# Kernel optimization log

Hardware: AMD Instinct MI355X
Metric: run time of the kernel (lower is better)

Reference implementation:

```python
import jax, jax.numpy as jnp
import numpy as np

B, T, D = 4, 4096, 1024
H = 16
DK = D // H
EPS = 1e-6


def _phi(x):
    return jax.nn.elu(x) + 1.0


def setup_inputs() -> dict:
    key = jax.random.key(0)
    ks = jax.random.split(key, 9)
    s = 1.0 / np.sqrt(D)
    return {
        "x": jax.random.normal(ks[0], (B, T, D), dtype=jnp.float32),
        "Wq": jax.random.uniform(ks[1], (D, D), jnp.float32, -s, s),
        "bq": jax.random.uniform(ks[2], (D,), jnp.float32, -s, s),
        "Wk": jax.random.uniform(ks[3], (D, D), jnp.float32, -s, s),
        "bk": jax.random.uniform(ks[4], (D,), jnp.float32, -s, s),
        "Wv": jax.random.uniform(ks[5], (D, D), jnp.float32, -s, s),
        "bv": jax.random.uniform(ks[6], (D,), jnp.float32, -s, s),
        "Wo": jax.random.uniform(ks[7], (D, D), jnp.float32, -s, s),
        "bo": jax.random.uniform(ks[8], (D,), jnp.float32, -s, s),
    }


def reference(x, Wq, bq, Wk, bk, Wv, bv, Wo, bo):
    Bq, Tq, _ = x.shape

    def heads(y):  # [B,T,D] -> [B,H,T,DK]
        return y.reshape(Bq, Tq, H, DK).transpose(0, 2, 1, 3)

    q = _phi(heads(x @ Wq.T + bq))
    k = _phi(heads(x @ Wk.T + bk))
    v = heads(x @ Wv.T + bv)

    # associative KV summary: [B,H,DK,DK]
    kv = jnp.einsum("bhtd,bhtm->bhdm", k, v)
    # normalizer: q . (sum_t k + eps), then +eps, reciprocal
    z = 1.0 / (jnp.einsum("bhtd,bhd->bht", q, k.sum(axis=2) + EPS) + EPS)
    out = jnp.einsum("bhtd,bhdm,bht->bhtm", q, kv, z)

    out = out.transpose(0, 2, 1, 3).reshape(Bq, Tq, -1)  # [B,T,D]
    return out @ Wo.T + bo
```

## Files before the change

kernel.cpp:

```cpp
#include <hip/hip_runtime.h>
#include <cstdint>
#include <cstddef>

typedef unsigned short u16;
typedef __bf16 bf16x8 __attribute__((ext_vector_type(8)));
typedef float  f32x4  __attribute__((ext_vector_type(4)));
typedef u16    u16x8v __attribute__((ext_vector_type(8)));
typedef u16    u16x4  __attribute__((ext_vector_type(4)));

#define EPS 1e-6f

__device__ __forceinline__ u16 f2bf(float f) {
  union { float f; unsigned int u; } v; v.f = f;
  unsigned int u = v.u + 0x7FFFu + ((v.u >> 16) & 1u);
  return (u16)(u >> 16);
}
__device__ __forceinline__ float bf2f(u16 h) {
  union { unsigned int u; float f; } v; v.u = ((unsigned int)h) << 16;
  return v.f;
}
__device__ __forceinline__ void async16(const void* g, void* l) {
  __builtin_amdgcn_global_load_lds(
      (const __attribute__((address_space(1))) void*)g,
      (__attribute__((address_space(3))) void*)l, 16, 0, 0);
}

__global__ __launch_bounds__(256) void cvt_bf16_kernel(
    const float* __restrict__ in, u16* __restrict__ out, int n8) {
  int i = blockIdx.x * 256 + threadIdx.x;
  if (i >= n8) return;
  const float4* p = (const float4*)in;
  float4 a = p[2 * (size_t)i], b = p[2 * (size_t)i + 1];
  u16x8v o;
  o[0] = f2bf(a.x); o[1] = f2bf(a.y); o[2] = f2bf(a.z); o[3] = f2bf(a.w);
  o[4] = f2bf(b.x); o[5] = f2bf(b.y); o[6] = f2bf(b.z); o[7] = f2bf(b.w);
  *(u16x8v*)(out + 8 * (size_t)i) = o;
}

__global__ __launch_bounds__(256) void cvt_w_kernel(
    const float* __restrict__ w0, const float* __restrict__ w1,
    const float* __restrict__ w2, const float* __restrict__ w3,
    u16* __restrict__ o0, u16* __restrict__ o1,
    u16* __restrict__ o2, u16* __restrict__ o3) {
  const int gb = blockIdx.x;
  const float* in = (gb < 512) ? w0 : (gb < 1024) ? w1 : (gb < 1536) ? w2 : w3;
  u16* out = (gb < 512) ? o0 : (gb < 1024) ? o1 : (gb < 1536) ? o2 : o3;
  const int i = (gb & 511) * 256 + threadIdx.x;
  const float4* p = (const float4*)in;
  float4 a = p[2 * (size_t)i], b = p[2 * (size_t)i + 1];
  u16x8v o;
  o[0] = f2bf(a.x); o[1] = f2bf(a.y); o[2] = f2bf(a.z); o[3] = f2bf(a.w);
  o[4] = f2bf(b.x); o[5] = f2bf(b.y); o[6] = f2bf(b.z); o[7] = f2bf(b.w);
  *(u16x8v*)(out + 8 * (size_t)i) = o;
}

template <int MODE>
__global__ __launch_bounds__(512) void gemm8p(
    const u16* __restrict__ A, const u16* __restrict__ Bw,
    const float* __restrict__ bias0, const float* __restrict__ bias1,
    const float* __restrict__ bias2,
    u16* __restrict__ O0, u16* __restrict__ O1, u16* __restrict__ O2,
    float* __restrict__ Of, int K) {
  __shared__ u16 sA[2][256 * 64];
  __shared__ u16 sB[2][256 * 64];

  const int tid = threadIdx.x, wave = tid >> 6, lane = tid & 63;
  const int bm = blockIdx.x * 256, bn = blockIdx.y * 256;
  const int wmh = (wave >> 2) * 64;
  const int wq  = (wave & 3) * 32;
  const int l15 = lane & 15, l4 = lane >> 4, l7 = lane & 7;

  f32x4 acc[8][4] = {};

  const int trow = tid >> 3;
  const int sch8 = ((tid & 7) ^ (trow & 7)) * 8;

#define STG_A(buf, qm, s, kt)                                                 \
  async16(A + (size_t)(bm + (s)*128 + (qm)*64 + trow) * K + (kt) + sch8,      \
          &sA[buf][(((qm)*128 + (s)*64) + wave * 8) * 64])
#define STG_B(buf, qn, s, kt)                                                 \
  async16(Bw + (size_t)(bn + ((s)*2 + (trow >> 5)) * 64 + (qn)*32 +           \
                        (trow & 31)) * K + (kt) + sch8,                       \
          &sB[buf][(((qn)*128 + (s)*64) + wave * 8) * 64])

  bf16x8 af[4][2], bq[2][2];

#define PH_READS(buf, qm, qn)                                                 \
  _Pragma("unroll") for (int m = 0; m < 4; m++)                               \
    _Pragma("unroll") for (int kk = 0; kk < 2; kk++)                          \
      af[m][kk] = *(const bf16x8*)&sA[buf][((qm)*128 + wmh + m * 16 + l15) * 64 \
                                           + ((kk * 4 + l4) ^ l7) * 8];       \
  _Pragma("unroll") for (int n = 0; n < 2; n++)                               \
    _Pragma("unroll") for (int kk = 0; kk < 2; kk++)                          \
      bq[n][kk] = *(const bf16x8*)&sB[buf][((qn)*128 + wq + n * 16 + l15) * 64 \
                                           + ((kk * 4 + l4) ^ l7) * 8];

#define PH_MFMA(qm, qn)                                                       \
  __builtin_amdgcn_s_barrier();                                               \
  asm volatile("s_waitcnt lgkmcnt(0)" ::: "memory");                          \
  __builtin_amdgcn_s_setprio(1);                                              \
  _Pragma("unroll") for (int kk = 0; kk < 2; kk++)                            \
    _Pragma("unroll") for (int m = 0; m < 4; m++)                             \
      _Pragma("unroll") for (int n = 0; n < 2; n++)                           \
        acc[(qm)*4 + m][(qn)*2 + n] = __builtin_amdgcn_mfma_f32_16x16x32_bf16(\
            af[m][kk], bq[n][kk], acc[(qm)*4 + m][(qn)*2 + n], 0, 0, 0);      \
  __builtin_amdgcn_s_setprio(0);                                              \
  __builtin_amdgcn_s_barrier();                                               \
  asm volatile("" ::: "memory");

  STG_A(0, 0, 0, 0);  STG_A(0, 0, 1, 0);
  STG_B(0, 0, 0, 0);  STG_B(0, 0, 1, 0);
  STG_A(0, 1, 0, 0);  STG_A(0, 1, 1, 0);
  STG_B(0, 1, 0, 0);  STG_B(0, 1, 1, 0);
  STG_A(1, 0, 0, 64); STG_A(1, 0, 1, 64);
  STG_B(1, 0, 0, 64); STG_B(1, 0, 1, 64);
  asm volatile("s_waitcnt vmcnt(4)" ::: "memory");
  __builtin_amdgcn_s_barrier();
  asm volatile("" ::: "memory");

  const int NT = K >> 6;
  const int NI = NT >> 1;
  for (int i = 0; i < NI; ++i) {
    const int kO  = (2 * i + 1) * 64;
    const int kE2 = (2 * i + 2) * 64;
    const int kO2 = (2 * i + 3) * 64;
    const bool gE2 = (2 * i + 2) < NT;
    const bool gO2 = (2 * i + 3) < NT;

    PH_READS(0, 0, 0);
    STG_A(1, 1, 0, kO); STG_A(1, 1, 1, kO);
    PH_MFMA(0, 0);
    PH_READS(0, 0, 1);
    STG_B(1, 1, 0, kO); STG_B(1, 1, 1, kO);
    PH_MFMA(0, 1);
    PH_READS(0, 1, 0);
    if (gE2) { STG_A(0, 0, 0, kE2); STG_A(0, 0, 1, kE2); }
    PH_MFMA(1, 0);
    PH_READS(0, 1, 1);
    if (gE2) {
      STG_B(0, 0, 0, kE2); STG_B(0, 0, 1, kE2);
      asm volatile("s_waitcnt vmcnt(4)" ::: "memory");
    } else {
      asm volatile("s_waitcnt vmcnt(0)" ::: "memory");
    }
    PH_MFMA(1, 1);
    PH_READS(1, 0, 0);
    if (gE2) { STG_A(0, 1, 0, kE2); STG_A(0, 1, 1, kE2); }
    PH_MFMA(0, 0);
    PH_READS(1, 0, 1);
    if (gE2) { STG_B(0, 1, 0, kE2); STG_B(0, 1, 1, kE2); }
    PH_MFMA(0, 1);
    PH_READS(1, 1, 0);
    if (gO2) { STG_A(1, 0, 0, kO2); STG_A(1, 0, 1, kO2); }
    PH_MFMA(1, 0);
    PH_READS(1, 1, 1);
    if (gO2) { STG_B(1, 0, 0, kO2); STG_B(1, 0, 1, kO2); }
    asm volatile("s_waitcnt vmcnt(4)" ::: "memory");
    PH_MFMA(1, 1);
  }
#undef STG_A
#undef STG_B
#undef PH_READS
#undef PH_MFMA

  const int wm = wmh * 2;
  const int wn = (wave & 3) * 64;
  const int r0 = l4 * 4, cc = l15;
  if constexpr (MODE == 1) {
    const int mat = blockIdx.y >> 2;
    u16* outp = (mat == 0) ? O0 : (mat == 1) ? O1 : O2;
    const float* bias = (mat == 0) ? bias0 : (mat == 1) ? bias1 : bias2;
    const int act = (mat < 2);
    const int colb = (blockIdx.y & 3) * 256;
    float bvv[4];
#pragma unroll
    for (int ni = 0; ni < 4; ni++) bvv[ni] = bias[colb + wn + ni * 16 + cc];
#pragma unroll
    for (int mi = 0; mi < 8; mi++) {
#pragma unroll
      for (int j = 0; j < 4; j++) {
        const int row = bm + wm + mi * 16 + r0 + j;
#pragma unroll
        for (int ni = 0; ni < 4; ni++) {
          const int col = colb + wn + ni * 16 + cc;
          float val = acc[mi][ni][j] + bvv[ni];
          if (act) val = (val > 0.f) ? (val + 1.f) : __expf(val);
          outp[(size_t)row * 1024 + col] = f2bf(val);
        }
      }
    }
  } else {
    float bvv[4];
#pragma unroll
    for (int ni = 0; ni < 4; ni++) bvv[ni] = bias0[bn + wn + ni * 16 + cc];
#pragma unroll
    for (int mi = 0; mi < 8; mi++) {
#pragma unroll
      for (int j = 0; j < 4; j++) {
        const int row = bm + wm + mi * 16 + r0 + j;
#pragma unroll
        for (int ni = 0; ni < 4; ni++) {
          const int col = bn + wn + ni * 16 + cc;
          Of[(size_t)row * 1024 + col] = acc[mi][ni][j] + bvv[ni];
        }
      }
    }
  }
}

__global__ __launch_bounds__(256) void kv_mfma_kernel(
    const u16* __restrict__ Kb, const u16* __restrict__ Vb,
    float* __restrict__ kv, float* __restrict__ ksum) {
  const int bh = blockIdx.y;
  const int chunk = blockIdx.x;
  const int b = bh >> 4, h = bh & 15;
  const int tid = threadIdx.x, wave = tid >> 6, lane = tid & 63;

  __shared__ u16 sKT[64 * 64];
  __shared__ u16 sVT[64 * 64];

  f32x4 acc[4] = {};
  f32x4 accs[4] = {};

  union { u16x8v u; bf16x8 b; } uo;
#pragma unroll
  for (int e = 0; e < 8; e++) uo.u[e] = 0x3F80;
  const bf16x8 ones = uo.b;

  const int half = tid >> 7;
  const int j    = tid & 127;
  const int tg   = j >> 3;
  const int dg   = j & 7;
  const u16* src = half ? Vb : Kb;
  u16* dst = half ? sVT : sKT;
  const int colb = (4 * tg + 8 * dg) & 63;

  const size_t rowBase = (size_t)b * 4096 + (size_t)chunk * 512;
  const size_t gbase = (rowBase + 4 * tg) * 1024 + (size_t)h * 64 + dg * 8;

  u16x8v pre[2][4];
#pragma unroll
  for (int s = 0; s < 4; s++)
    pre[0][s] = *(const u16x8v*)(src + gbase + (size_t)s * 1024);

#pragma unroll
  for (int st = 0; st < 8; st++) {
    const int cb = st & 1;
    __syncthreads();
#pragma unroll
    for (int e = 0; e < 8; e++) {
      u16x4 w;
      w[0] = pre[cb][0][e]; w[1] = pre[cb][1][e];
      w[2] = pre[cb][2][e]; w[3] = pre[cb][3][e];
      *(u16x4*)&dst[(dg * 8 + e) * 64 + colb] = w;
    }
    if (st + 1 < 8) {
      const size_t nb = gbase + (size_t)(st + 1) * 64 * 1024;
#pragma unroll
      for (int s = 0; s < 4; s++)
        pre[cb ^ 1][s] = *(const u16x8v*)(src + nb + (size_t)s * 1024);
    }
    __syncthreads();

#pragma unroll
    for (int kst = 0; kst < 2; kst++) {
      const int q8 = kst * 32 + (lane >> 4) * 8;
      bf16x8 bfrag;
      {
        const int rr = wave * 16 + (lane & 15);
        const int c = (q8 + 8 * (rr >> 3)) & 63;
        bfrag = *(const bf16x8*)&sVT[rr * 64 + c];
      }
#pragma unroll
      for (int i = 0; i < 4; i++) {
        const int rr = i * 16 + (lane & 15);
        const int c = (q8 + 8 * (rr >> 3)) & 63;
        const bf16x8 afrag = *(const bf16x8*)&sKT[rr * 64 + c];
        acc[i] = __builtin_amdgcn_mfma_f32_16x16x32_bf16(afrag, bfrag, acc[i], 0, 0, 0);
        if (wave == 0)
          accs[i] = __builtin_amdgcn_mfma_f32_16x16x32_bf16(afrag, ones, accs[i], 0, 0, 0);
      }
    }
  }

  const int r0 = (lane >> 4) * 4, cc = lane & 15;
  float* kvp = kv + (size_t)bh * 4096;
#pragma unroll
  for (int i = 0; i < 4; i++)
#pragma unroll
    for (int jj = 0; jj < 4; jj++)
      atomicAdd(&kvp[(size_t)(i * 16 + r0 + jj) * 64 + wave * 16 + cc], acc[i][jj]);
  if (wave == 0 && cc == 0) {
#pragma unroll
    for (int i = 0; i < 4; i++)
#pragma unroll
      for (int jj = 0; jj < 4; jj++)
        atomicAdd(&ksum[(size_t)bh * 64 + i * 16 + r0 + jj], accs[i][jj]);
  }
}

#define QST 80
__global__ __launch_bounds__(256) void attn_apply_kernel(
    const u16* __restrict__ Qb, const float* __restrict__ kv,
    const float* __restrict__ ksum, u16* __restrict__ attn) {
  const int bh = blockIdx.y;
  const int tt = blockIdx.x;
  const int b = bh >> 4, h = bh & 15;
  const int tid = threadIdx.x, wave = tid >> 6, lane = tid & 63;

  __shared__ u16 skvT[64 * QST];
  __shared__ u16 sq[64 * QST];
  __shared__ float sz[64];
  __shared__ float sks[64];

  if (tid < 64) sks[tid] = ksum[(size_t)bh * 64 + tid] + EPS;

  const float* kvp = kv + (size_t)bh * 4096;
  for (int i = tid; i < 4096; i += 256) {
    const int dd = i >> 6, mm = i & 63;
    skvT[mm * QST + dd] = f2bf(kvp[i]);
  }
  const size_t qbase = ((size_t)b * 4096 + (size_t)tt * 64) * 1024 + h * 64;
  for (int i = tid; i < 4096; i += 256) {
    const int r = i >> 6, dd = i & 63;
    sq[r * QST + dd] = Qb[qbase + (size_t)r * 1024 + dd];
  }
  __syncthreads();

  if (tid < 64) {
    float za = 0.f;
#pragma unroll
    for (int j = 0; j < 64; j++) {
      const int dd = (j + tid) & 63;
      za += bf2f(sq[tid * QST + dd]) * sks[dd];
    }
    sz[tid] = 1.f / (za + EPS);
  }
  __syncthreads();

  f32x4 acc[4] = {};
#pragma unroll
  for (int ks2 = 0; ks2 < 2; ks2++) {
    const bf16x8 a = *(const bf16x8*)&sq[(wave * 16 + (lane & 15)) * QST + ks2 * 32 + (lane >> 4) * 8];
#pragma unroll
    for (int ni = 0; ni < 4; ni++) {
      const bf16x8 bv = *(const bf16x8*)&skvT[(ni * 16 + (lane & 15)) * QST + ks2 * 32 + (lane >> 4) * 8];
      acc[ni] = __builtin_amdgcn_mfma_f32_16x16x32_bf16(a, bv, acc[ni], 0, 0, 0);
    }
  }

  const int r0 = (lane >> 4) * 4, cc = lane & 15;
#pragma unroll
  for (int ni = 0; ni < 4; ni++) {
#pragma unroll
    for (int j = 0; j < 4; j++) {
      const int r = wave * 16 + r0 + j;
      const int c = ni * 16 + cc;
      const float val = acc[ni][j] * sz[r];
      attn[qbase + (size_t)r * 1024 + c] = f2bf(val);
    }
  }
}

extern "C" void kernel_launch(void* const* d_in, const int* in_sizes, int n_in,
                              void* d_out, int out_size, void* d_ws, size_t ws_size,
                              hipStream_t stream) {
  (void)in_sizes; (void)n_in; (void)out_size; (void)ws_size;
  const float* x  = (const float*)d_in[0];
  const float* Wq = (const float*)d_in[1];
  const float* bq = (const float*)d_in[2];
  const float* Wk = (const float*)d_in[3];
  const float* bk = (const float*)d_in[4];
  const float* Wv = (const float*)d_in[5];
  const float* bv = (const float*)d_in[6];
  const float* Wo = (const float*)d_in[7];
  const float* bo = (const float*)d_in[8];

  char* ws = (char*)d_ws;
  u16* xb    = (u16*)ws;  ws += 33554432;
  u16* wqkvb = (u16*)ws;  ws += 6291456;
  u16* wob   = (u16*)ws;  ws += 2097152;
  u16* Vb    = (u16*)ws;  ws += 33554432;
  u16* attn  = (u16*)ws;  ws += 33554432;
  float* kvb  = (float*)ws; ws += 1048576;
  float* ksum = (float*)ws; ws += 16384;

  u16* Qb = (u16*)d_out;
  u16* Kb = Qb + 16777216;

  hipMemsetAsync(kvb, 0, 1048576 + 16384, stream);

  cvt_bf16_kernel<<<8192, 256, 0, stream>>>(x, xb, 2097152);
  cvt_w_kernel<<<2048, 256, 0, stream>>>(Wq, Wk, Wv, Wo,
                                         wqkvb, wqkvb + 1048576, wqkvb + 2097152, wob);

  gemm8p<1><<<dim3(64, 12), 512, 0, stream>>>(
      xb, wqkvb, bq, bk, bv, Qb, Kb, Vb, nullptr, 1024);

  kv_mfma_kernel<<<dim3(8, 64), dim3(256), 0, stream>>>(Kb, Vb, kvb, ksum);
  attn_apply_kernel<<<dim3(64, 64), dim3(256), 0, stream>>>(Qb, kvb, ksum, attn);

  gemm8p<0><<<dim3(64, 4), 512, 0, stream>>>(
      attn, wob, bo, nullptr, nullptr, nullptr, nullptr, nullptr,
      (float*)d_out, 1024);
}
```

Before: 338.0 us.

## Restructure GEMM main loop into four phases with full B-fragment reuse

Changes the bf16 MFMA GEMM inner loop from eight phases per double-tile to four. Each phase now loads all four B fragments once and reuses them across a 4x4 MFMA block, which halves the barriers per tile and removes redundant LDS reads of B. Global-to-LDS prefetches are regrouped and the vmcnt waits move into the phase epilogue, with a peeled final iteration that drains the pipeline. It adds sched_barrier and raises register pressure from the larger B fragment set, and the staged-load ordering is fragile if the wait counts do not match.

```diff
diff --git a/kernel.cpp b/kernel.cpp
--- a/kernel.cpp
+++ b/kernel.cpp
@@ -55,7 +55,7 @@
 }
 
 template <int MODE>
-__global__ __launch_bounds__(512) void gemm8p(
+__global__ __launch_bounds__(512) void gemm4p(
     const u16* __restrict__ A, const u16* __restrict__ Bw,
     const float* __restrict__ bias0, const float* __restrict__ bias1,
     const float* __restrict__ bias2,
@@ -83,85 +83,91 @@
                         (trow & 31)) * K + (kt) + sch8,                       \
           &sB[buf][(((qn)*128 + (s)*64) + wave * 8) * 64])
 
-  bf16x8 af[4][2], bq[2][2];
-
-#define PH_READS(buf, qm, qn)                                                 \
+  bf16x8 af[4][2], bq[4][2];
+
+#define RD_A(buf, qm)                                                         \
   _Pragma("unroll") for (int m = 0; m < 4; m++)                               \
     _Pragma("unroll") for (int kk = 0; kk < 2; kk++)                          \
       af[m][kk] = *(const bf16x8*)&sA[buf][((qm)*128 + wmh + m * 16 + l15) * 64 \
-                                           + ((kk * 4 + l4) ^ l7) * 8];       \
-  _Pragma("unroll") for (int n = 0; n < 2; n++)                               \
+                                           + ((kk * 4 + l4) ^ l7) * 8];
+#define RD_B(buf)                                                             \
+  _Pragma("unroll") for (int nf = 0; nf < 4; nf++)                            \
     _Pragma("unroll") for (int kk = 0; kk < 2; kk++)                          \
-      bq[n][kk] = *(const bf16x8*)&sB[buf][((qn)*128 + wq + n * 16 + l15) * 64 \
-                                           + ((kk * 4 + l4) ^ l7) * 8];
-
-#define PH_MFMA(qm, qn)                                                       \
+      bq[nf][kk] = *(const bf16x8*)&sB[buf][((nf >> 1) * 128 + wq +           \
+                                            (nf & 1) * 16 + l15) * 64 +       \
+                                           ((kk * 4 + l4) ^ l7) * 8];
+
+#define WAITV(n) asm volatile("s_waitcnt vmcnt(" #n ")" ::: "memory")
+
+#define PH_EXEC(qm, NW)                                                       \
   __builtin_amdgcn_s_barrier();                                               \
   asm volatile("s_waitcnt lgkmcnt(0)" ::: "memory");                          \
+  __builtin_amdgcn_sched_barrier(0);                                          \
   __builtin_amdgcn_s_setprio(1);                                              \
   _Pragma("unroll") for (int kk = 0; kk < 2; kk++)                            \
     _Pragma("unroll") for (int m = 0; m < 4; m++)                             \
-      _Pragma("unroll") for (int n = 0; n < 2; n++)                           \
-        acc[(qm)*4 + m][(qn)*2 + n] = __builtin_amdgcn_mfma_f32_16x16x32_bf16(\
-            af[m][kk], bq[n][kk], acc[(qm)*4 + m][(qn)*2 + n], 0, 0, 0);      \
+      _Pragma("unroll") for (int nf = 0; nf < 4; nf++)                        \
+        acc[(qm)*4 + m][nf] = __builtin_amdgcn_mfma_f32_16x16x32_bf16(        \
+            af[m][kk], bq[nf][kk], acc[(qm)*4 + m][nf], 0, 0, 0);             \
   __builtin_amdgcn_s_setprio(0);                                              \
+  WAITV(NW);                                                                  \
   __builtin_amdgcn_s_barrier();                                               \
   asm volatile("" ::: "memory");
 
+#define ITER_BODY(kO, kE2, kO2, hasT2, hasT3, W0, W1, W2, W3)                 \
+                                          \
+  RD_B(0); RD_A(0, 0);                                                        \
+  STG_A(1, 1, 0, kO); STG_A(1, 1, 1, kO);               \
+  PH_EXEC(0, W0);                                                             \
+                                                          \
+  RD_A(0, 1);                                                                 \
+  if (hasT2) {                                                                \
+    STG_B(0, 0, 0, kE2); STG_B(0, 0, 1, kE2);                                 \
+    STG_B(0, 1, 0, kE2); STG_B(0, 1, 1, kE2);                       \
+    STG_A(0, 0, 0, kE2); STG_A(0, 0, 1, kE2);                      \
+  }                                                                           \
+  PH_EXEC(1, W1);                                                             \
+                                          \
+  RD_B(1); RD_A(1, 0);                                                        \
+  if (hasT2) { STG_A(0, 1, 0, kE2); STG_A(0, 1, 1, kE2); }         \
+  PH_EXEC(0, W2);                                                             \
+                                                          \
+  RD_A(1, 1);                                                                 \
+  if (hasT3) {                                                                \
+    STG_B(1, 0, 0, kO2); STG_B(1, 0, 1, kO2);                                 \
+    STG_B(1, 1, 0, kO2); STG_B(1, 1, 1, kO2);                       \
+    STG_A(1, 0, 0, kO2); STG_A(1, 0, 1, kO2);                      \
+  }                                                                           \
+  PH_EXEC(1, W3);
+
+  STG_B(0, 0, 0, 0);  STG_B(0, 0, 1, 0);  STG_B(0, 1, 0, 0);  STG_B(0, 1, 1, 0);
   STG_A(0, 0, 0, 0);  STG_A(0, 0, 1, 0);
-  STG_B(0, 0, 0, 0);  STG_B(0, 0, 1, 0);
   STG_A(0, 1, 0, 0);  STG_A(0, 1, 1, 0);
-  STG_B(0, 1, 0, 0);  STG_B(0, 1, 1, 0);
+  STG_B(1, 0, 0, 64); STG_B(1, 0, 1, 64); STG_B(1, 1, 0, 64); STG_B(1, 1, 1, 64);
   STG_A(1, 0, 0, 64); STG_A(1, 0, 1, 64);
-  STG_B(1, 0, 0, 64); STG_B(1, 0, 1, 64);
-  asm volatile("s_waitcnt vmcnt(4)" ::: "memory");
+  WAITV(6);
   __builtin_amdgcn_s_barrier();
   asm volatile("" ::: "memory");
 
   const int NT = K >> 6;
   const int NI = NT >> 1;
-  for (int i = 0; i < NI; ++i) {
+  for (int i = 0; i < NI - 1; ++i) {
     const int kO  = (2 * i + 1) * 64;
     const int kE2 = (2 * i + 2) * 64;
     const int kO2 = (2 * i + 3) * 64;
-    const bool gE2 = (2 * i + 2) < NT;
-    const bool gO2 = (2 * i + 3) < NT;
-
-    PH_READS(0, 0, 0);
-    STG_A(1, 1, 0, kO); STG_A(1, 1, 1, kO);
-    PH_MFMA(0, 0);
-    PH_READS(0, 0, 1);
-    STG_B(1, 1, 0, kO); STG_B(1, 1, 1, kO);
-    PH_MFMA(0, 1);
-    PH_READS(0, 1, 0);
-    if (gE2) { STG_A(0, 0, 0, kE2); STG_A(0, 0, 1, kE2); }
-    PH_MFMA(1, 0);
-    PH_READS(0, 1, 1);
-    if (gE2) {
-      STG_B(0, 0, 0, kE2); STG_B(0, 0, 1, kE2);
-      asm volatile("s_waitcnt vmcnt(4)" ::: "memory");
-    } else {
-      asm volatile("s_waitcnt vmcnt(0)" ::: "memory");
-    }
-    PH_MFMA(1, 1);
-    PH_READS(1, 0, 0);
-    if (gE2) { STG_A(0, 1, 0, kE2); STG_A(0, 1, 1, kE2); }
-    PH_MFMA(0, 0);
-    PH_READS(1, 0, 1);
-    if (gE2) { STG_B(0, 1, 0, kE2); STG_B(0, 1, 1, kE2); }
-    PH_MFMA(0, 1);
-    PH_READS(1, 1, 0);
-    if (gO2) { STG_A(1, 0, 0, kO2); STG_A(1, 0, 1, kO2); }
-    PH_MFMA(1, 0);
-    PH_READS(1, 1, 1);
-    if (gO2) { STG_B(1, 0, 0, kO2); STG_B(1, 0, 1, kO2); }
-    asm volatile("s_waitcnt vmcnt(4)" ::: "memory");
-    PH_MFMA(1, 1);
+    ITER_BODY(kO, kE2, kO2, true, true, 8, 8, 8, 8);
+  }
+  {
+    const int kO = (NT - 1) * 64;
+    ITER_BODY(kO, 0, 0, false, false, 8, 2, 0, 0);
   }
 #undef STG_A
 #undef STG_B
-#undef PH_READS
-#undef PH_MFMA
+#undef RD_A
+#undef RD_B
+#undef WAITV
+#undef PH_EXEC
+#undef ITER_BODY
 
   const int wm = wmh * 2;
   const int wn = (wave & 3) * 64;
@@ -394,13 +400,13 @@
   cvt_w_kernel<<<2048, 256, 0, stream>>>(Wq, Wk, Wv, Wo,
                                          wqkvb, wqkvb + 1048576, wqkvb + 2097152, wob);
 
-  gemm8p<1><<<dim3(64, 12), 512, 0, stream>>>(
+  gemm4p<1><<<dim3(64, 12), 512, 0, stream>>>(
       xb, wqkvb, bq, bk, bv, Qb, Kb, Vb, nullptr, 1024);
 
   kv_mfma_kernel<<<dim3(8, 64), dim3(256), 0, stream>>>(Kb, Vb, kvb, ksum);
   attn_apply_kernel<<<dim3(64, 64), dim3(256), 0, stream>>>(Qb, kvb, ksum, attn);
 
-  gemm8p<0><<<dim3(64, 4), 512, 0, stream>>>(
+  gemm4p<0><<<dim3(64, 4), 512, 0, stream>>>(
       attn, wob, bo, nullptr, nullptr, nullptr, nullptr, nullptr,
       (float*)d_out, 1024);
 }
```

Result: faster. 319.7 us (-5.4%).
